# Performance work log

Measured on AMD Instinct MI355X. Metric: run time of the kernel, lower is better.

The kernel has to match this reference:

```python
import jax, jax.numpy as jnp
import numpy as np

MAX_STEPS = 32
EPSILON = 0.01
LN_EPS = 1e-5


def setup_inputs() -> dict:
    key = jax.random.key(0)
    ks = jax.random.split(key, 8)
    B, D, H = 4096, 512, 2048
    std = 0.02  # larger than torch init so the loop does not trivially converge
    return {
        "z_init": jax.random.normal(ks[0], (B, D), jnp.float32),
        "ln1_g": jnp.ones((D,), jnp.float32),
        "ln1_b": jnp.zeros((D,), jnp.float32),
        "w1": jax.random.normal(ks[1], (D, H), jnp.float32) * std,
        "b1": jnp.zeros((H,), jnp.float32),
        "w2": jax.random.normal(ks[2], (H, D), jnp.float32) * std,
        "b2": jnp.zeros((D,), jnp.float32),
        "ln2_g": jnp.ones((D,), jnp.float32),
        "ln2_b": jnp.zeros((D,), jnp.float32),
        "w3": jax.random.normal(ks[3], (D, H), jnp.float32) * std,
        "b3": jnp.zeros((H,), jnp.float32),
        "w4": jax.random.normal(ks[4], (H, D), jnp.float32) * std,
        "b4": jnp.zeros((D,), jnp.float32),
        "clf_w": jax.random.normal(ks[5], (D, 1), jnp.float32) * 0.02,
        "clf_b": jnp.zeros((1,), jnp.float32),
    }


def _layernorm(x, g, b):
    m = jnp.mean(x, axis=-1, keepdims=True)
    v = jnp.var(x, axis=-1, keepdims=True)
    return (x - m) * jax.lax.rsqrt(v + LN_EPS) * g + b


def reference(z_init, ln1_g, ln1_b, w1, b1, w2, b2, ln2_g, ln2_b, w3, b3, w4, b4,
              clf_w, clf_b):
    def block(z):
        h = _layernorm(z, ln1_g, ln1_b)
        h = jax.nn.gelu(h @ w1 + b1, approximate=False)
        h = h @ w2 + b2
        h = _layernorm(h, ln2_g, ln2_b)
        h = jax.nn.gelu(h @ w3 + b3, approximate=False)
        return h @ w4 + b4

    def step(carry, _):
        z_t, mask = carry
        delta = block(z_t)                       # [B, D]
        z_next = z_t + delta
        dist = jnp.linalg.norm(delta, axis=-1)   # ||z_next - z_t||_2
        mask = mask | (dist < EPSILON)
        z_t = jnp.where(mask[:, None], z_t, z_next)
        return (z_t, mask), None

    B = z_init.shape[0]
    init = (z_init, jnp.zeros((B,), jnp.bool_))
    (z_t, converged_mask), _ = jax.lax.scan(step, init, None, length=MAX_STEPS)
    logits = z_t @ clf_w + clf_b                 # [B, 1]
    return logits, converged_mask, z_t
```

## Files before the change

kernel.cpp:

```cpp
#include <hip/hip_runtime.h>

#define B_ROWS  4096
#define D_DIM   512
#define H_DIM   2048
#define N_STEPS 32
#define EPS_CONV 0.01f
#define LN_EPSF  1e-5f

typedef __attribute__((ext_vector_type(4))) float f32x4;
typedef __attribute__((ext_vector_type(8))) _Float16 h16x8;
typedef unsigned short ushort_t;
typedef unsigned int uint32;

__device__ __forceinline__ float wave_reduce_sum(float v) {
#pragma unroll
  for (int o = 32; o > 0; o >>= 1) v += __shfl_down(v, o, 64);
  return v;
}

__device__ __forceinline__ float gelu_exact(float v) {
  return 0.5f * v * (1.0f + erff(v * 0.7071067811865476f));
}

__device__ __forceinline__ ushort_t h_bits(_Float16 h) {
  union { _Float16 f; ushort_t u; } c; c.f = h; return c.u;
}

__device__ __forceinline__ size_t amap_h(int row, int k, int K) {
  return ((size_t)((row >> 4) * (K >> 5) + (k >> 5)) << 10) +
         ((((((k >> 3) & 3) << 4) + (row & 15))) << 3) + (k & 7);
}

__global__ __launch_bounds__(256)
void ln_pack_kernel(const float* in, const float* in2, const float* g,
                    const float* b, ushort_t* outp) {
  const int row = blockIdx.x;
  const int t = threadIdx.x;
  float2 v = ((const float2*)(in + (size_t)row * D_DIM))[t];
  if (in2 != nullptr) {
    const float2 w = ((const float2*)(in2 + (size_t)row * D_DIM))[t];
    v.x += w.x; v.y += w.y;
  }
  float s  = v.x + v.y;
  float sq = v.x * v.x + v.y * v.y;
  s  = wave_reduce_sum(s);
  sq = wave_reduce_sum(sq);
  __shared__ float sd1[4], sd2[4], mb[2];
  const int lane = t & 63, wid = t >> 6;
  if (lane == 0) { sd1[wid] = s; sd2[wid] = sq; }
  __syncthreads();
  if (t == 0) {
    float st = sd1[0] + sd1[1] + sd1[2] + sd1[3];
    float qt = sd2[0] + sd2[1] + sd2[2] + sd2[3];
    float mean = st * (1.0f / (float)D_DIM);
    float var  = qt * (1.0f / (float)D_DIM) - mean * mean;
    mb[0] = mean;
    mb[1] = rsqrtf(var + LN_EPSF);
  }
  __syncthreads();
  const float mean = mb[0], rstd = mb[1];
  const float2 gv = ((const float2*)g)[t];
  const float2 bv = ((const float2*)b)[t];
  const float r0 = (v.x - mean) * rstd * gv.x + bv.x;
  const float r1 = (v.y - mean) * rstd * gv.y + bv.y;
  const _Float16 h0 = (_Float16)r0, h1 = (_Float16)r1;
  const _Float16 l0 = (_Float16)((r0 - (float)h0) * 1024.0f);
  const _Float16 l1 = (_Float16)((r1 - (float)h1) * 1024.0f);
  const size_t base = amap_h(row, 2 * t, D_DIM);
  union { _Float16 f[2]; uint32 u; } ph, pl;
  ph.f[0] = h0; ph.f[1] = h1;
  pl.f[0] = l0; pl.f[1] = l1;
  *(uint32*)(outp + base) = ph.u;
  *(uint32*)(outp + base + 512) = pl.u;
}

__global__ __launch_bounds__(256)
void transpose_split_kernel(const float* __restrict__ w,
                            ushort_t* __restrict__ wp, int K, int N) {
  __shared__ float t[32][33];
  const int tx = threadIdx.x;
  const int ty = threadIdx.y;
  const int n_base = blockIdx.x * 32;
  const int k_base = blockIdx.y * 32;
#pragma unroll
  for (int r = 0; r < 4; ++r)
    t[ty + r * 8][tx] = w[(size_t)(k_base + ty + r * 8) * N + n_base + tx];
  __syncthreads();
#pragma unroll
  for (int r = 0; r < 4; ++r) {
    const int n = n_base + ty + r * 8;
    const int k = k_base + tx;
    const float v = t[tx][ty + r * 8];
    const _Float16 hi = (_Float16)v;
    const _Float16 lo = (_Float16)((v - (float)hi) * 1024.0f);
    const size_t base = amap_h(n, k, K);
    wp[base] = h_bits(hi);
    wp[base + 512] = h_bits(lo);
  }
}

template <bool OUT_PACK>
__global__ __launch_bounds__(256, 2)
void gemm_direct(const ushort_t* __restrict__ Ah, const ushort_t* __restrict__ Wh,
                 const float* __restrict__ bias, ushort_t* __restrict__ Cp,
                 float* __restrict__ C0, float* __restrict__ C1,
                 int M, int N, int K, int kc) {
  const int KT = K >> 5;
  const int NKT = kc >> 5;

  const int tid = threadIdx.x;
  const int lane = tid & 63;
  const int wid = tid >> 6;
  const int q = lane >> 4;
  const int l16 = lane & 15;
  const int wm = wid >> 1;
  const int wn = wid & 1;

  const int m0 = blockIdx.x * 128;
  const int n0 = blockIdx.y * 64;
  const int kt0 = blockIdx.z * NKT;

  const ushort_t* pa[4];
#pragma unroll
  for (int i = 0; i < 4; ++i) {
    const int tm = (m0 >> 4) + wm * 4 + i;
    pa[i] = Ah + ((size_t)(tm * KT + kt0) << 10) + lane * 8;
  }
  const ushort_t* pb[2];
#pragma unroll
  for (int j = 0; j < 2; ++j) {
    const int tn = (n0 >> 4) + wn * 2 + j;
    pb[j] = Wh + ((size_t)(tn * KT + kt0) << 10) + lane * 8;
  }

  f32x4 acc_h[4][2], acc_m[4][2];
#pragma unroll
  for (int i = 0; i < 4; ++i)
#pragma unroll
    for (int j = 0; j < 2; ++j) {
      acc_h[i][j] = (f32x4){0.f, 0.f, 0.f, 0.f};
      acc_m[i][j] = (f32x4){0.f, 0.f, 0.f, 0.f};
    }

  h16x8 a0h[4], a0l[4], a1h[4], a1l[4];
  h16x8 b0h[2], b0l[2], b1h[2], b1l[2];

#define LDF(p, off) (*(const h16x8*)((p) + (off)))
#define MFMA_BANK(AH, AL, BH, BL)                                             \
  _Pragma("unroll") for (int i = 0; i < 4; ++i)                               \
  _Pragma("unroll") for (int j = 0; j < 2; ++j) {                             \
    acc_h[i][j] = __builtin_amdgcn_mfma_f32_16x16x32_f16(AH[i], BH[j],        \
                                                         acc_h[i][j], 0, 0, 0);\
    acc_m[i][j] = __builtin_amdgcn_mfma_f32_16x16x32_f16(AL[i], BH[j],        \
                                                         acc_m[i][j], 0, 0, 0);\
    acc_m[i][j] = __builtin_amdgcn_mfma_f32_16x16x32_f16(AH[i], BL[j],        \
                                                         acc_m[i][j], 0, 0, 0);\
  }

#pragma unroll
  for (int i = 0; i < 4; ++i) { a0h[i] = LDF(pa[i], 0); a0l[i] = LDF(pa[i], 512); }
#pragma unroll
  for (int j = 0; j < 2; ++j) { b0h[j] = LDF(pb[j], 0); b0l[j] = LDF(pb[j], 512); }

  for (int kt = 0; kt < NKT - 2; kt += 2) {
#pragma unroll
    for (int i = 0; i < 4; ++i) { a1h[i] = LDF(pa[i], 1024); a1l[i] = LDF(pa[i], 1536); }
#pragma unroll
    for (int j = 0; j < 2; ++j) { b1h[j] = LDF(pb[j], 1024); b1l[j] = LDF(pb[j], 1536); }
    MFMA_BANK(a0h, a0l, b0h, b0l)
#pragma unroll
    for (int i = 0; i < 4; ++i) pa[i] += 2048;
#pragma unroll
    for (int j = 0; j < 2; ++j) pb[j] += 2048;
#pragma unroll
    for (int i = 0; i < 4; ++i) { a0h[i] = LDF(pa[i], 0); a0l[i] = LDF(pa[i], 512); }
#pragma unroll
    for (int j = 0; j < 2; ++j) { b0h[j] = LDF(pb[j], 0); b0l[j] = LDF(pb[j], 512); }
    MFMA_BANK(a1h, a1l, b1h, b1l)
  }
#pragma unroll
  for (int i = 0; i < 4; ++i) { a1h[i] = LDF(pa[i], 1024); a1l[i] = LDF(pa[i], 1536); }
#pragma unroll
  for (int j = 0; j < 2; ++j) { b1h[j] = LDF(pb[j], 1024); b1l[j] = LDF(pb[j], 1536); }
  MFMA_BANK(a0h, a0l, b0h, b0l)
  MFMA_BANK(a1h, a1l, b1h, b1l)
#undef MFMA_BANK
#undef LDF

#pragma unroll
  for (int i = 0; i < 4; ++i) {
    const int row = m0 + wm * 64 + i * 16 + q * 4;
#pragma unroll
    for (int j = 0; j < 2; ++j) {
      const int col = n0 + wn * 32 + j * 16 + l16;
      if (OUT_PACK) {
        const float bv = bias[col];
#pragma unroll
        for (int r = 0; r < 4; ++r) {
          const float v = gelu_exact(acc_h[i][j][r] +
                                     acc_m[i][j][r] * (1.0f / 1024.0f) + bv);
          const _Float16 hi = (_Float16)v;
          const _Float16 lo = (_Float16)((v - (float)hi) * 1024.0f);
          const size_t base = amap_h(row + r, col, N);
          Cp[base] = h_bits(hi);
          Cp[base + 512] = h_bits(lo);
        }
      } else {
        float* C = (blockIdx.z == 0) ? C0 : C1;
        const float bv = (blockIdx.z == 0) ? bias[col] : 0.0f;
#pragma unroll
        for (int r = 0; r < 4; ++r) {
          C[(size_t)(row + r) * N + col] =
              acc_h[i][j][r] + acc_m[i][j][r] * (1.0f / 1024.0f) + bv;
        }
      }
    }
  }
}

__global__ __launch_bounds__(256)
void update_kernel(float* __restrict__ z, const float* __restrict__ d0,
                   const float* __restrict__ d1, int* __restrict__ mask) {
  const int row = blockIdx.x;
  const int t = threadIdx.x;
  float2 d = ((const float2*)(d0 + (size_t)row * D_DIM))[t];
  const float2 e = ((const float2*)(d1 + (size_t)row * D_DIM))[t];
  d.x += e.x; d.y += e.y;
  float sq = d.x * d.x + d.y * d.y;
  sq = wave_reduce_sum(sq);
  __shared__ float sd[4];
  __shared__ int frozen_sh;
  const int lane = t & 63, wid = t >> 6;
  if (lane == 0) sd[wid] = sq;
  __syncthreads();
  if (t == 0) {
    const float dist = sqrtf(sd[0] + sd[1] + sd[2] + sd[3]);
    const int m = mask[row];
    const int newly = (dist < EPS_CONV) ? 1 : 0;
    if (!m && newly) mask[row] = 1;
    frozen_sh = m | newly;
  }
  __syncthreads();
  if (!frozen_sh) {
    float2* zp = (float2*)(z + (size_t)row * D_DIM);
    float2 zv = zp[t];
    zv.x += d.x; zv.y += d.y;
    zp[t] = zv;
  }
}

__global__ __launch_bounds__(256)
void final_kernel(const float* __restrict__ z, const float* __restrict__ clf_w,
                  const float* __restrict__ clf_b, const int* __restrict__ mask,
                  float* __restrict__ logits, float* __restrict__ maskf) {
  const int row = blockIdx.x;
  const int t = threadIdx.x;
  const float2 zv = ((const float2*)(z + (size_t)row * D_DIM))[t];
  const float2 wv = ((const float2*)clf_w)[t];
  float s = zv.x * wv.x + zv.y * wv.y;
  s = wave_reduce_sum(s);
  __shared__ float sd[4];
  const int lane = t & 63, wid = t >> 6;
  if (lane == 0) sd[wid] = s;
  __syncthreads();
  if (t == 0) {
    logits[row] = sd[0] + sd[1] + sd[2] + sd[3] + clf_b[0];
    maskf[row] = mask[row] ? 1.0f : 0.0f;
  }
}

__global__ void init_kernel(const float* __restrict__ z_init,
                            float* __restrict__ z, int* __restrict__ mask,
                            int n) {
  const int i = blockIdx.x * blockDim.x + threadIdx.x;
  if (i < n) z[i] = z_init[i];
  if (i < B_ROWS) mask[i] = 0;
}

__global__ __launch_bounds__(256)
void ln_f32_kernel(const float* __restrict__ in, const float* __restrict__ g,
                   const float* __restrict__ b, float* __restrict__ out) {
  const int row = blockIdx.x;
  const int t = threadIdx.x;
  const float2 v = ((const float2*)(in + (size_t)row * D_DIM))[t];
  float s = v.x + v.y, sq = v.x * v.x + v.y * v.y;
  s = wave_reduce_sum(s); sq = wave_reduce_sum(sq);
  __shared__ float sd1[4], sd2[4], mb[2];
  const int lane = t & 63, wid = t >> 6;
  if (lane == 0) { sd1[wid] = s; sd2[wid] = sq; }
  __syncthreads();
  if (t == 0) {
    float st = sd1[0] + sd1[1] + sd1[2] + sd1[3];
    float qt = sd2[0] + sd2[1] + sd2[2] + sd2[3];
    float mean = st / (float)D_DIM;
    float var = qt / (float)D_DIM - mean * mean;
    mb[0] = mean; mb[1] = rsqrtf(var + LN_EPSF);
  }
  __syncthreads();
  const float mean = mb[0], rstd = mb[1];
  const float2 gv = ((const float2*)g)[t];
  const float2 bv = ((const float2*)b)[t];
  float2 r;
  r.x = (v.x - mean) * rstd * gv.x + bv.x;
  r.y = (v.y - mean) * rstd * gv.y + bv.y;
  ((float2*)(out + (size_t)row * D_DIM))[t] = r;
}

__global__ __launch_bounds__(256)
void update_f32_kernel(float* __restrict__ z, const float* __restrict__ delta,
                       int* __restrict__ mask) {
  const int row = blockIdx.x;
  const int t = threadIdx.x;
  const float2 d = ((const float2*)(delta + (size_t)row * D_DIM))[t];
  float sq = d.x * d.x + d.y * d.y;
  sq = wave_reduce_sum(sq);
  __shared__ float sd[4];
  __shared__ int frozen_sh;
  const int lane = t & 63, wid = t >> 6;
  if (lane == 0) sd[wid] = sq;
  __syncthreads();
  if (t == 0) {
    const float dist = sqrtf(sd[0] + sd[1] + sd[2] + sd[3]);
    const int m = mask[row];
    const int newly = (dist < EPS_CONV) ? 1 : 0;
    if (!m && newly) mask[row] = 1;
    frozen_sh = m | newly;
  }
  __syncthreads();
  if (!frozen_sh) {
    float2* zp = (float2*)(z + (size_t)row * D_DIM);
    float2 zv = zp[t];
    zv.x += d.x; zv.y += d.y;
    zp[t] = zv;
  }
}

template <int BM, int BN>
__global__ __launch_bounds__(256)
void gemm_fp32_fallback(const float* __restrict__ A, const float* __restrict__ W,
                        const float* __restrict__ bias, float* __restrict__ C,
                        int M, int N, int K, int do_gelu) {
  constexpr int BK = 8;
  constexpr int TM = BM / 16;
  constexpr int TN = BN / 16;
  __shared__ float As[BK][BM];
  __shared__ float Bs[BK][BN];
  const int tid = threadIdx.x;
  const int m0 = blockIdx.x * BM;
  const int n0 = blockIdx.y * BN;
  const int ty = tid >> 4, tx = tid & 15;
  float acc[TM][TN];
#pragma unroll
  for (int i = 0; i < TM; ++i)
#pragma unroll
    for (int j = 0; j < TN; ++j) acc[i][j] = 0.0f;
  for (int k0 = 0; k0 < K; k0 += BK) {
    if constexpr (BM == 128) {
      const int row = tid >> 1, col = (tid & 1) * 4;
      const float4 a = *(const float4*)(A + (size_t)(m0 + row) * K + k0 + col);
      As[col + 0][row] = a.x; As[col + 1][row] = a.y;
      As[col + 2][row] = a.z; As[col + 3][row] = a.w;
    } else {
      const int row = tid >> 2, col = (tid & 3) * 2;
      const float2 a = *(const float2*)(A + (size_t)(m0 + row) * K + k0 + col);
      As[col + 0][row] = a.x; As[col + 1][row] = a.y;
    }
    {
      const int row = tid >> 5, col = (tid & 31) * 4;
      const float4 w = *(const float4*)(W + (size_t)(k0 + row) * N + n0 + col);
      *(float4*)(&Bs[row][col]) = w;
    }
    __syncthreads();
#pragma unroll
    for (int kk = 0; kk < BK; ++kk) {
      float a[TM], b[TN];
#pragma unroll
      for (int i = 0; i < TM; i += 4)
        *(float4*)(a + i) = *(const float4*)(&As[kk][ty * TM + i]);
#pragma unroll
      for (int j = 0; j < TN; j += 4)
        *(float4*)(b + j) = *(const float4*)(&Bs[kk][tx * TN + j]);
#pragma unroll
      for (int i = 0; i < TM; ++i)
#pragma unroll
        for (int j = 0; j < TN; ++j) acc[i][j] = fmaf(a[i], b[j], acc[i][j]);
    }
    __syncthreads();
  }
  float bv[TN];
#pragma unroll
  for (int j = 0; j < TN; ++j) bv[j] = bias[n0 + tx * TN + j];
#pragma unroll
  for (int i = 0; i < TM; ++i) {
    const int r = m0 + ty * TM + i;
#pragma unroll
    for (int j = 0; j < TN; j += 4) {
      float4 v;
      v.x = acc[i][j + 0] + bv[j + 0]; v.y = acc[i][j + 1] + bv[j + 1];
      v.z = acc[i][j + 2] + bv[j + 2]; v.w = acc[i][j + 3] + bv[j + 3];
      if (do_gelu) {
        v.x = gelu_exact(v.x); v.y = gelu_exact(v.y);
        v.z = gelu_exact(v.z); v.w = gelu_exact(v.w);
      }
      *(float4*)(C + (size_t)r * N + n0 + tx * TN + j) = v;
    }
  }
}

extern "C" void kernel_launch(void* const* d_in, const int* in_sizes, int n_in,
                              void* d_out, int out_size, void* d_ws,
                              size_t ws_size, hipStream_t stream) {
  const float* z_init = (const float*)d_in[0];
  const float* ln1_g  = (const float*)d_in[1];
  const float* ln1_b  = (const float*)d_in[2];
  const float* w1     = (const float*)d_in[3];
  const float* b1     = (const float*)d_in[4];
  const float* w2     = (const float*)d_in[5];
  const float* b2     = (const float*)d_in[6];
  const float* ln2_g  = (const float*)d_in[7];
  const float* ln2_b  = (const float*)d_in[8];
  const float* w3     = (const float*)d_in[9];
  const float* b3     = (const float*)d_in[10];
  const float* w4     = (const float*)d_in[11];
  const float* b4     = (const float*)d_in[12];
  const float* clf_w  = (const float*)d_in[13];
  const float* clf_b  = (const float*)d_in[14];

  float* out    = (float*)d_out;
  float* logits = out;
  float* maskf  = out + B_ROWS;
  float* z      = out + 2 * B_ROWS;

  const size_t BD = (size_t)B_ROWS * D_DIM;
  const size_t BH = (size_t)B_ROWS * H_DIM;
  const size_t WSZ = (size_t)D_DIM * H_DIM;

  ushort_t* xh  = (ushort_t*)d_ws;
  ushort_t* hp  = xh + BD * 2;
  float*    y   = (float*)(hp + BH * 2);
  float*    p1  = y + BD;
  ushort_t* w1p = (ushort_t*)(p1 + BD);
  ushort_t* w2p = w1p + WSZ * 2;
  ushort_t* w3p = w2p + WSZ * 2;
  ushort_t* w4p = w3p + WSZ * 2;
  int*     mask = (int*)(w4p + WSZ * 2);
  const size_t need = (uintptr_t)((char*)(mask + B_ROWS) - (char*)d_ws) + 256;

  init_kernel<<<(int)((BD + 255) / 256), 256, 0, stream>>>(z_init, z, mask,
                                                           (int)BD);

  if (ws_size >= need) {
    const dim3 tb(32, 8);
    transpose_split_kernel<<<dim3(H_DIM / 32, D_DIM / 32), tb, 0, stream>>>(w1, w1p, D_DIM, H_DIM);
    transpose_split_kernel<<<dim3(D_DIM / 32, H_DIM / 32), tb, 0, stream>>>(w2, w2p, H_DIM, D_DIM);
    transpose_split_kernel<<<dim3(H_DIM / 32, D_DIM / 32), tb, 0, stream>>>(w3, w3p, D_DIM, H_DIM);
    transpose_split_kernel<<<dim3(D_DIM / 32, H_DIM / 32), tb, 0, stream>>>(w4, w4p, H_DIM, D_DIM);

    const dim3 g_up(B_ROWS / 128, H_DIM / 64, 1);
    const dim3 g_dn(B_ROWS / 128, D_DIM / 64, 2);
    for (int s = 0; s < N_STEPS; ++s) {
      ln_pack_kernel<<<B_ROWS, 256, 0, stream>>>(z, nullptr, ln1_g, ln1_b, xh);
      gemm_direct<true><<<g_up, 256, 0, stream>>>(
          xh, w1p, b1, hp, nullptr, nullptr, B_ROWS, H_DIM, D_DIM, D_DIM);
      gemm_direct<false><<<g_dn, 256, 0, stream>>>(
          hp, w2p, b2, nullptr, y, p1, B_ROWS, D_DIM, H_DIM, H_DIM / 2);
      ln_pack_kernel<<<B_ROWS, 256, 0, stream>>>(y, p1, ln2_g, ln2_b, xh);
      gemm_direct<true><<<g_up, 256, 0, stream>>>(
          xh, w3p, b3, hp, nullptr, nullptr, B_ROWS, H_DIM, D_DIM, D_DIM);
      gemm_direct<false><<<g_dn, 256, 0, stream>>>(
          hp, w4p, b4, nullptr, y, p1, B_ROWS, D_DIM, H_DIM, H_DIM / 2);
      update_kernel<<<B_ROWS, 256, 0, stream>>>(z, y, p1, mask);
    }
  } else {
    float* x  = (float*)d_ws;
    float* yf = x + BD;
    float* h  = yf + BD;
    int* mask_fb = (int*)(h + BH);
    mask = mask_fb;
    const dim3 g_up(B_ROWS / 128, H_DIM / 128);
    const dim3 g_dn(B_ROWS / 64, D_DIM / 128);
    for (int s = 0; s < N_STEPS; ++s) {
      ln_f32_kernel<<<B_ROWS, 256, 0, stream>>>(z, ln1_g, ln1_b, x);
      gemm_fp32_fallback<128, 128><<<g_up, 256, 0, stream>>>(x, w1, b1, h, B_ROWS, H_DIM, D_DIM, 1);
      gemm_fp32_fallback<64, 128><<<g_dn, 256, 0, stream>>>(h, w2, b2, yf, B_ROWS, D_DIM, H_DIM, 0);
      ln_f32_kernel<<<B_ROWS, 256, 0, stream>>>(yf, ln2_g, ln2_b, x);
      gemm_fp32_fallback<128, 128><<<g_up, 256, 0, stream>>>(x, w3, b3, h, B_ROWS, H_DIM, D_DIM, 1);
      gemm_fp32_fallback<64, 128><<<g_dn, 256, 0, stream>>>(h, w4, b4, yf, B_ROWS, D_DIM, H_DIM, 0);
      update_f32_kernel<<<B_ROWS, 256, 0, stream>>>(z, yf, mask);
    }
  }
  final_kernel<<<B_ROWS, 256, 0, stream>>>(z, clf_w, clf_b, mask, logits, maskf);
}
```

Baseline: 6.207 ms.

## Switch GEMMs to 32x32x16 MFMA tiles with 128x128 blocks and 4-way split-K

Rewrites the packed fp16 hi/lo operand layout for 32-row tiles and moves the GEMMs from 16x16x32 to 32x32x16 MFMA instructions. Each block now covers 128x128 outputs, and the down-projection is split four ways along K into four partial buffers. The LayerNorm and update kernels sum those four partials. The larger MFMA tiles give more reuse per operand load. The cost is extra partial-buffer traffic in the down-projections and a different accumulator register layout.

```diff
diff --git a/kernel.cpp b/kernel.cpp
--- a/kernel.cpp
+++ b/kernel.cpp
@@ -7,7 +7,7 @@
 #define EPS_CONV 0.01f
 #define LN_EPSF  1e-5f
 
-typedef __attribute__((ext_vector_type(4))) float f32x4;
+typedef __attribute__((ext_vector_type(16))) float f32x16;
 typedef __attribute__((ext_vector_type(8))) _Float16 h16x8;
 typedef unsigned short ushort_t;
 typedef unsigned int uint32;
@@ -26,21 +26,21 @@
   union { _Float16 f; ushort_t u; } c; c.f = h; return c.u;
 }
 
-__device__ __forceinline__ size_t amap_h(int row, int k, int K) {
-  return ((size_t)((row >> 4) * (K >> 5) + (k >> 5)) << 10) +
-         ((((((k >> 3) & 3) << 4) + (row & 15))) << 3) + (k & 7);
-}
-
-__global__ __launch_bounds__(256)
-void ln_pack_kernel(const float* in, const float* in2, const float* g,
-                    const float* b, ushort_t* outp) {
+__device__ __forceinline__ size_t amap32(int row, int k, int K) {
+  return ((size_t)((row >> 5) * (K >> 4) + (k >> 4)) << 10) +
+         ((size_t)((((k >> 3) & 1) << 5) | (row & 31)) << 3) + (k & 7);
+}
+
+__global__ __launch_bounds__(256)
+void ln_pack_kernel(const float* in0, const float* in1, const float* in2,
+                    const float* in3, const float* g, const float* b,
+                    ushort_t* outp) {
   const int row = blockIdx.x;
   const int t = threadIdx.x;
-  float2 v = ((const float2*)(in + (size_t)row * D_DIM))[t];
-  if (in2 != nullptr) {
-    const float2 w = ((const float2*)(in2 + (size_t)row * D_DIM))[t];
-    v.x += w.x; v.y += w.y;
-  }
+  float2 v = ((const float2*)(in0 + (size_t)row * D_DIM))[t];
+  if (in1) { const float2 w = ((const float2*)(in1 + (size_t)row * D_DIM))[t]; v.x += w.x; v.y += w.y; }
+  if (in2) { const float2 w = ((const float2*)(in2 + (size_t)row * D_DIM))[t]; v.x += w.x; v.y += w.y; }
+  if (in3) { const float2 w = ((const float2*)(in3 + (size_t)row * D_DIM))[t]; v.x += w.x; v.y += w.y; }
   float s  = v.x + v.y;
   float sq = v.x * v.x + v.y * v.y;
   s  = wave_reduce_sum(s);
@@ -66,7 +66,7 @@
   const _Float16 h0 = (_Float16)r0, h1 = (_Float16)r1;
   const _Float16 l0 = (_Float16)((r0 - (float)h0) * 1024.0f);
   const _Float16 l1 = (_Float16)((r1 - (float)h1) * 1024.0f);
-  const size_t base = amap_h(row, 2 * t, D_DIM);
+  const size_t base = amap32(row, 2 * t, D_DIM);
   union { _Float16 f[2]; uint32 u; } ph, pl;
   ph.f[0] = h0; ph.f[1] = h1;
   pl.f[0] = l0; pl.f[1] = l1;
@@ -93,7 +93,7 @@
     const float v = t[tx][ty + r * 8];
     const _Float16 hi = (_Float16)v;
     const _Float16 lo = (_Float16)((v - (float)hi) * 1024.0f);
-    const size_t base = amap_h(n, k, K);
+    const size_t base = amap32(n, k, K);
     wp[base] = h_bits(hi);
     wp[base + 512] = h_bits(lo);
   }
@@ -101,85 +101,84 @@
 
 template <bool OUT_PACK>
 __global__ __launch_bounds__(256, 2)
-void gemm_direct(const ushort_t* __restrict__ Ah, const ushort_t* __restrict__ Wh,
-                 const float* __restrict__ bias, ushort_t* __restrict__ Cp,
-                 float* __restrict__ C0, float* __restrict__ C1,
-                 int M, int N, int K, int kc) {
-  const int KT = K >> 5;
-  const int NKT = kc >> 5;
+void gemm32(const ushort_t* __restrict__ Ah, const ushort_t* __restrict__ Wh,
+            const float* __restrict__ bias, ushort_t* __restrict__ Cp,
+            float* __restrict__ C0, float* __restrict__ C1,
+            float* __restrict__ C2, float* __restrict__ C3,
+            int M, int N, int K, int kc) {
+  const int KT = K >> 4;
+  const int NKT = kc >> 4;
 
   const int tid = threadIdx.x;
   const int lane = tid & 63;
   const int wid = tid >> 6;
-  const int q = lane >> 4;
-  const int l16 = lane & 15;
   const int wm = wid >> 1;
   const int wn = wid & 1;
 
   const int m0 = blockIdx.x * 128;
-  const int n0 = blockIdx.y * 64;
-  const int kt0 = blockIdx.z * NKT;
-
-  const ushort_t* pa[4];
-#pragma unroll
-  for (int i = 0; i < 4; ++i) {
-    const int tm = (m0 >> 4) + wm * 4 + i;
-    pa[i] = Ah + ((size_t)(tm * KT + kt0) << 10) + lane * 8;
+  const int n0 = blockIdx.y * 128;
+  const int kz0 = blockIdx.z * NKT;
+
+  const ushort_t* pa[2];
+#pragma unroll
+  for (int i = 0; i < 2; ++i) {
+    const int tm = (m0 >> 5) + wm * 2 + i;
+    pa[i] = Ah + ((size_t)(tm * KT + kz0) << 10) + lane * 8;
   }
   const ushort_t* pb[2];
 #pragma unroll
   for (int j = 0; j < 2; ++j) {
-    const int tn = (n0 >> 4) + wn * 2 + j;
-    pb[j] = Wh + ((size_t)(tn * KT + kt0) << 10) + lane * 8;
-  }
-
-  f32x4 acc_h[4][2], acc_m[4][2];
-#pragma unroll
-  for (int i = 0; i < 4; ++i)
+    const int tn = (n0 >> 5) + wn * 2 + j;
+    pb[j] = Wh + ((size_t)(tn * KT + kz0) << 10) + lane * 8;
+  }
+
+  f32x16 acc_h[2][2], acc_m[2][2];
+#pragma unroll
+  for (int i = 0; i < 2; ++i)
 #pragma unroll
     for (int j = 0; j < 2; ++j) {
-      acc_h[i][j] = (f32x4){0.f, 0.f, 0.f, 0.f};
-      acc_m[i][j] = (f32x4){0.f, 0.f, 0.f, 0.f};
-    }
-
-  h16x8 a0h[4], a0l[4], a1h[4], a1l[4];
+      acc_h[i][j] = (f32x16)(0.0f);
+      acc_m[i][j] = (f32x16)(0.0f);
+    }
+
+  h16x8 a0h[2], a0l[2], a1h[2], a1l[2];
   h16x8 b0h[2], b0l[2], b1h[2], b1l[2];
 
 #define LDF(p, off) (*(const h16x8*)((p) + (off)))
-#define MFMA_BANK(AH, AL, BH, BL)                                             \
-  _Pragma("unroll") for (int i = 0; i < 4; ++i)                               \
-  _Pragma("unroll") for (int j = 0; j < 2; ++j) {                             \
-    acc_h[i][j] = __builtin_amdgcn_mfma_f32_16x16x32_f16(AH[i], BH[j],        \
+#define MFMA_BANK(AH, AL, BH, BL)                                              \
+  _Pragma("unroll") for (int i = 0; i < 2; ++i)                                \
+  _Pragma("unroll") for (int j = 0; j < 2; ++j) {                              \
+    acc_h[i][j] = __builtin_amdgcn_mfma_f32_32x32x16_f16(AH[i], BH[j],         \
                                                          acc_h[i][j], 0, 0, 0);\
-    acc_m[i][j] = __builtin_amdgcn_mfma_f32_16x16x32_f16(AL[i], BH[j],        \
+    acc_m[i][j] = __builtin_amdgcn_mfma_f32_32x32x16_f16(AL[i], BH[j],         \
                                                          acc_m[i][j], 0, 0, 0);\
-    acc_m[i][j] = __builtin_amdgcn_mfma_f32_16x16x32_f16(AH[i], BL[j],        \
+    acc_m[i][j] = __builtin_amdgcn_mfma_f32_32x32x16_f16(AH[i], BL[j],         \
                                                          acc_m[i][j], 0, 0, 0);\
   }
 
 #pragma unroll
-  for (int i = 0; i < 4; ++i) { a0h[i] = LDF(pa[i], 0); a0l[i] = LDF(pa[i], 512); }
+  for (int i = 0; i < 2; ++i) { a0h[i] = LDF(pa[i], 0); a0l[i] = LDF(pa[i], 512); }
 #pragma unroll
   for (int j = 0; j < 2; ++j) { b0h[j] = LDF(pb[j], 0); b0l[j] = LDF(pb[j], 512); }
 
   for (int kt = 0; kt < NKT - 2; kt += 2) {
 #pragma unroll
-    for (int i = 0; i < 4; ++i) { a1h[i] = LDF(pa[i], 1024); a1l[i] = LDF(pa[i], 1536); }
+    for (int i = 0; i < 2; ++i) { a1h[i] = LDF(pa[i], 1024); a1l[i] = LDF(pa[i], 1536); }
 #pragma unroll
     for (int j = 0; j < 2; ++j) { b1h[j] = LDF(pb[j], 1024); b1l[j] = LDF(pb[j], 1536); }
     MFMA_BANK(a0h, a0l, b0h, b0l)
 #pragma unroll
-    for (int i = 0; i < 4; ++i) pa[i] += 2048;
+    for (int i = 0; i < 2; ++i) pa[i] += 2048;
 #pragma unroll
     for (int j = 0; j < 2; ++j) pb[j] += 2048;
 #pragma unroll
-    for (int i = 0; i < 4; ++i) { a0h[i] = LDF(pa[i], 0); a0l[i] = LDF(pa[i], 512); }
+    for (int i = 0; i < 2; ++i) { a0h[i] = LDF(pa[i], 0); a0l[i] = LDF(pa[i], 512); }
 #pragma unroll
     for (int j = 0; j < 2; ++j) { b0h[j] = LDF(pb[j], 0); b0l[j] = LDF(pb[j], 512); }
     MFMA_BANK(a1h, a1l, b1h, b1l)
   }
 #pragma unroll
-  for (int i = 0; i < 4; ++i) { a1h[i] = LDF(pa[i], 1024); a1l[i] = LDF(pa[i], 1536); }
+  for (int i = 0; i < 2; ++i) { a1h[i] = LDF(pa[i], 1024); a1l[i] = LDF(pa[i], 1536); }
 #pragma unroll
   for (int j = 0; j < 2; ++j) { b1h[j] = LDF(pb[j], 1024); b1l[j] = LDF(pb[j], 1536); }
   MFMA_BANK(a0h, a0l, b0h, b0l)
@@ -187,31 +186,29 @@
 #undef MFMA_BANK
 #undef LDF
 
-#pragma unroll
-  for (int i = 0; i < 4; ++i) {
-    const int row = m0 + wm * 64 + i * 16 + q * 4;
+  const int cq = (lane >> 5) * 4;
+  const int col_l = lane & 31;
+#pragma unroll
+  for (int i = 0; i < 2; ++i) {
 #pragma unroll
     for (int j = 0; j < 2; ++j) {
-      const int col = n0 + wn * 32 + j * 16 + l16;
-      if (OUT_PACK) {
-        const float bv = bias[col];
-#pragma unroll
-        for (int r = 0; r < 4; ++r) {
-          const float v = gelu_exact(acc_h[i][j][r] +
-                                     acc_m[i][j][r] * (1.0f / 1024.0f) + bv);
+      const int colb = n0 + wn * 64 + j * 32 + col_l;
+      const float bv = (OUT_PACK || blockIdx.z == 0) ? bias[colb] : 0.0f;
+#pragma unroll
+      for (int r = 0; r < 16; ++r) {
+        const int row = m0 + wm * 64 + i * 32 + (r & 3) + 8 * (r >> 2) + cq;
+        float v = acc_h[i][j][r] + acc_m[i][j][r] * (1.0f / 1024.0f) + bv;
+        if (OUT_PACK) {
+          v = gelu_exact(v);
           const _Float16 hi = (_Float16)v;
           const _Float16 lo = (_Float16)((v - (float)hi) * 1024.0f);
-          const size_t base = amap_h(row + r, col, N);
+          const size_t base = amap32(row, colb, N);
           Cp[base] = h_bits(hi);
           Cp[base + 512] = h_bits(lo);
-        }
-      } else {
-        float* C = (blockIdx.z == 0) ? C0 : C1;
-        const float bv = (blockIdx.z == 0) ? bias[col] : 0.0f;
-#pragma unroll
-        for (int r = 0; r < 4; ++r) {
-          C[(size_t)(row + r) * N + col] =
-              acc_h[i][j][r] + acc_m[i][j][r] * (1.0f / 1024.0f) + bv;
+        } else {
+          float* C = (blockIdx.z == 0) ? C0 : (blockIdx.z == 1) ? C1
+                    : (blockIdx.z == 2) ? C2 : C3;
+          C[(size_t)row * N + colb] = v;
         }
       }
     }
@@ -220,12 +217,14 @@
 
 __global__ __launch_bounds__(256)
 void update_kernel(float* __restrict__ z, const float* __restrict__ d0,
-                   const float* __restrict__ d1, int* __restrict__ mask) {
+                   const float* __restrict__ d1, const float* __restrict__ d2,
+                   const float* __restrict__ d3, int* __restrict__ mask) {
   const int row = blockIdx.x;
   const int t = threadIdx.x;
   float2 d = ((const float2*)(d0 + (size_t)row * D_DIM))[t];
-  const float2 e = ((const float2*)(d1 + (size_t)row * D_DIM))[t];
-  d.x += e.x; d.y += e.y;
+  { const float2 e = ((const float2*)(d1 + (size_t)row * D_DIM))[t]; d.x += e.x; d.y += e.y; }
+  { const float2 e = ((const float2*)(d2 + (size_t)row * D_DIM))[t]; d.x += e.x; d.y += e.y; }
+  { const float2 e = ((const float2*)(d3 + (size_t)row * D_DIM))[t]; d.x += e.x; d.y += e.y; }
   float sq = d.x * d.x + d.y * d.y;
   sq = wave_reduce_sum(sq);
   __shared__ float sd[4];
@@ -437,9 +436,11 @@
 
   ushort_t* xh  = (ushort_t*)d_ws;
   ushort_t* hp  = xh + BD * 2;
-  float*    y   = (float*)(hp + BH * 2);
-  float*    p1  = y + BD;
-  ushort_t* w1p = (ushort_t*)(p1 + BD);
+  float*    y0  = (float*)(hp + BH * 2);
+  float*    y1  = y0 + BD;
+  float*    y2  = y1 + BD;
+  float*    y3  = y2 + BD;
+  ushort_t* w1p = (ushort_t*)(y3 + BD);
   ushort_t* w2p = w1p + WSZ * 2;
   ushort_t* w3p = w2p + WSZ * 2;
   ushort_t* w4p = w3p + WSZ * 2;
@@ -456,20 +457,26 @@
     transpose_split_kernel<<<dim3(H_DIM / 32, D_DIM / 32), tb, 0, stream>>>(w3, w3p, D_DIM, H_DIM);
     transpose_split_kernel<<<dim3(D_DIM / 32, H_DIM / 32), tb, 0, stream>>>(w4, w4p, H_DIM, D_DIM);
 
-    const dim3 g_up(B_ROWS / 128, H_DIM / 64, 1);
-    const dim3 g_dn(B_ROWS / 128, D_DIM / 64, 2);
+    const dim3 g_up(B_ROWS / 128, H_DIM / 128, 1);
+    const dim3 g_dn(B_ROWS / 128, D_DIM / 128, 4);
     for (int s = 0; s < N_STEPS; ++s) {
-      ln_pack_kernel<<<B_ROWS, 256, 0, stream>>>(z, nullptr, ln1_g, ln1_b, xh);
-      gemm_direct<true><<<g_up, 256, 0, stream>>>(
-          xh, w1p, b1, hp, nullptr, nullptr, B_ROWS, H_DIM, D_DIM, D_DIM);
-      gemm_direct<false><<<g_dn, 256, 0, stream>>>(
-          hp, w2p, b2, nullptr, y, p1, B_ROWS, D_DIM, H_DIM, H_DIM / 2);
-      ln_pack_kernel<<<B_ROWS, 256, 0, stream>>>(y, p1, ln2_g, ln2_b, xh);
-      gemm_direct<true><<<g_up, 256, 0, stream>>>(
-          xh, w3p, b3, hp, nullptr, nullptr, B_ROWS, H_DIM, D_DIM, D_DIM);
-      gemm_direct<false><<<g_dn, 256, 0, stream>>>(
-          hp, w4p, b4, nullptr, y, p1, B_ROWS, D_DIM, H_DIM, H_DIM / 2);
-      update_kernel<<<B_ROWS, 256, 0, stream>>>(z, y, p1, mask);
+      ln_pack_kernel<<<B_ROWS, 256, 0, stream>>>(z, nullptr, nullptr, nullptr,
+                                                 ln1_g, ln1_b, xh);
+      gemm32<true><<<g_up, 256, 0, stream>>>(
+          xh, w1p, b1, hp, nullptr, nullptr, nullptr, nullptr,
+          B_ROWS, H_DIM, D_DIM, D_DIM);
+      gemm32<false><<<g_dn, 256, 0, stream>>>(
+          hp, w2p, b2, nullptr, y0, y1, y2, y3,
+          B_ROWS, D_DIM, H_DIM, H_DIM / 4);
+      ln_pack_kernel<<<B_ROWS, 256, 0, stream>>>(y0, y1, y2, y3,
+                                                 ln2_g, ln2_b, xh);
+      gemm32<true><<<g_up, 256, 0, stream>>>(
+          xh, w3p, b3, hp, nullptr, nullptr, nullptr, nullptr,
+          B_ROWS, H_DIM, D_DIM, D_DIM);
+      gemm32<false><<<g_dn, 256, 0, stream>>>(
+          hp, w4p, b4, nullptr, y0, y1, y2, y3,
+          B_ROWS, D_DIM, H_DIM, H_DIM / 4);
+      update_kernel<<<B_ROWS, 256, 0, stream>>>(z, y0, y1, y2, y3, mask);
     }
   } else {
     float* x  = (float*)d_ws;
```

Measured after the change: 5.998 ms. 1.03x faster.
